# Kernel tuning notes

Measured on AMD Instinct MI355X. Metric: run time of the kernel, lower is better.

## Reference

```python
import jax, jax.numpy as jnp
import numpy as np

N = 100000      # nodes
E = 800000      # edges (nnz of sparse adj)
D_IN = 128      # input feature dim
H = 64          # hidden_units
EMB = 32        # embsize
N_IDX = 50000   # gathered output rows
EPS = 1e-05     # BatchNormalization epsilon


def spmm(rows, cols, vals, x):
    # out[i] = sum_{e: rows[e]==i} vals[e] * x[cols[e]]  == sparse A @ x
    return jax.ops.segment_sum(vals[:, None] * x[cols], rows, num_segments=N)


def batchnorm(x, gamma, beta):
    # training-mode BN over node (batch) axis, matching Keras BatchNormalization
    m = jnp.mean(x, axis=0)
    v = jnp.var(x, axis=0)
    return (x - m) * jax.lax.rsqrt(v + EPS) * gamma + beta


def setup_inputs() -> dict:
    key = jax.random.key(0)
    ks = jax.random.split(key, 16)
    def w(k, fan_in, shape):
        return jax.random.normal(k, shape, dtype=jnp.float32) / np.sqrt(fan_in)
    inp = {
        "features": jax.random.normal(ks[0], (N, D_IN), dtype=jnp.float32),
        "rows": jax.random.randint(ks[1], (E,), 0, N),
        "cols": jax.random.randint(ks[2], (E,), 0, N),
        "vals": jax.random.uniform(ks[3], (E,), dtype=jnp.float32),
        "idx": jax.random.randint(ks[4], (N_IDX,), 0, N),
        # layer 0 (Dense with bias since l==0)
        "Wn0": w(ks[5], D_IN, (D_IN, H)), "bn0": jnp.zeros((H,), jnp.float32),
        "Wg0": w(ks[6], D_IN, (D_IN, H)), "bg0": jnp.zeros((H,), jnp.float32),
        "ab0": jnp.zeros((H,), jnp.float32),  # BiasLayer after SpMM
        "g0": jnp.ones((H,), jnp.float32), "b0": jnp.zeros((H,), jnp.float32),
        # layer 1 (no Dense bias)
        "Wn1": w(ks[7], H, (H, H)),
        "Wg1": w(ks[8], H, (H, H)),
        "ab1": jnp.zeros((H,), jnp.float32),
        "g1": jnp.ones((H,), jnp.float32), "b1": jnp.zeros((H,), jnp.float32),
        # conv_last block (Dense use_bias=False)
        "WnL": w(ks[9], H, (H, EMB)),
        "WgL": w(ks[10], H, (H, EMB)),
        "abL": jnp.zeros((EMB,), jnp.float32),
    }
    return inp


def reference(features, rows, cols, vals, idx,
              Wn0, bn0, Wg0, bg0, ab0, g0, b0,
              Wn1, Wg1, ab1, g1, b1,
              WnL, WgL, abL):
    x = features
    # SAGE layer 0
    x_node = x @ Wn0 + bn0
    x_neigh = x @ Wg0 + bg0
    agg = spmm(rows, cols, vals, x_neigh) + ab0
    x = jax.nn.relu(batchnorm(x_node + agg, g0, b0))
    # SAGE layer 1
    x_node = x @ Wn1
    x_neigh = x @ Wg1
    agg = spmm(rows, cols, vals, x_neigh) + ab1
    x = jax.nn.relu(batchnorm(x_node + agg, g1, b1))
    # conv_last projection to embsize
    x_node = x @ WnL
    x_neigh = x @ WgL
    agg = spmm(rows, cols, vals, x_neigh) + abL
    x = x_node + agg
    return x[idx]
```

## Files before the change

kernel.cpp:

```cpp
#include <hip/hip_runtime.h>

#define NNODES 100000
#define NEDGES 800000
#define DIN    128
#define HID    64
#define EMB    32
#define NIDX   50000
#define BN_EPS 1e-5f

#define NCHK 64
#define EC   (NEDGES / NCHK)
#define NB   ((NNODES + 63) / 64)
#define PF   16
#define NBF  ((NB + PF - 1) / PF)

typedef __attribute__((ext_vector_type(8))) short short8;
typedef __attribute__((ext_vector_type(4))) float f32x4;

__device__ inline unsigned short f2bf(float f) {
    unsigned u = __float_as_uint(f);
    unsigned r = u + 0x7FFFu + ((u >> 16) & 1u);
    return (unsigned short)(r >> 16);
}
__device__ inline float bf2f_lo(unsigned u) { return __uint_as_float(u << 16); }
__device__ inline float bf2f_hi(unsigned u) { return __uint_as_float(u & 0xffff0000u); }


__device__ inline void pack_seg(const float* __restrict__ Wn, const float* __restrict__ Wg,
                                unsigned short* __restrict__ Wp, int HOUT, int l2nt, int f) {
    int j = f & 7, lane = (f >> 3) & 63, g = f >> 9;
    int tt = g & ((1 << l2nt) - 1), kb = g >> l2nt;
    int k = kb * 32 + ((lane >> 4) * 8) + j;
    int nn = tt * 16 + (lane & 15);
    float v = (nn < HOUT) ? Wn[k * HOUT + nn] : Wg[k * HOUT + (nn - HOUT)];
    Wp[f] = f2bf(v);
}


__global__ __launch_bounds__(256) void histpack_k(
    const int* __restrict__ rows, int* __restrict__ Bcnt4, int* __restrict__ bTot,
    const int* __restrict__ idx, int* __restrict__ mark,
    const float* Wn0, const float* Wg0, const float* Wn1,
    const float* Wg1, const float* WnL, const float* WgL,
    unsigned short* Wp0, unsigned short* Wp1, unsigned short* WpL, int MB)
{
    int blk = blockIdx.x;
    int t = threadIdx.x;
    if (blk >= NCHK + MB) {
        int f = (blk - NCHK - MB) * 256 + t;
        if (f < 16384)      pack_seg(Wn0, Wg0, Wp0, 64, 3, f);
        else if (f < 24576) pack_seg(Wn1, Wg1, Wp1, 64, 3, f - 16384);
        else if (f < 28672) pack_seg(WnL, WgL, WpL, 32, 2, f - 24576);
        return;
    }
    if (blk >= NCHK) {
        int j = (blk - NCHK) * 256 + t;
        if (j < NIDX) mark[idx[j]] = 1;
        return;
    }
    __shared__ int hist[NB];
    for (int b = t; b < NB; b += 256) hist[b] = 0;
    __syncthreads();
    const int* rbase = rows + blk * EC;
    for (int i4 = t; i4 < EC / 4; i4 += 256) {
        int4 r4 = *(const int4*)&rbase[i4 * 4];
        atomicAdd(&hist[r4.x >> 6], 1);
        atomicAdd(&hist[r4.y >> 6], 1);
        atomicAdd(&hist[r4.z >> 6], 1);
        atomicAdd(&hist[r4.w >> 6], 1);
    }
    __syncthreads();
    for (int b = t; b < NB; b += 256) {
        int h = hist[b];
        Bcnt4[blk * NB + b] = h;
        if (h) atomicAdd(&bTot[b], h);
    }
}

__global__ __launch_bounds__(256) void scan_k(
    const int* __restrict__ Bcnt4, int* __restrict__ BcntT,
    const int* __restrict__ bTot, int* __restrict__ bBase)
{
    int t = threadIdx.x;
    if (blockIdx.x < 7) {
        int b = blockIdx.x * 256 + t;
        if (b >= NB) return;
        int run = 0;
        for (int c = 0; c < NCHK; c++) {
            BcntT[c * NB + b] = run;
            run += Bcnt4[c * NB + b];
        }
        return;
    }
    __shared__ int s[256];
    int v[7], loc = 0;
#pragma unroll
    for (int i = 0; i < 7; i++) {
        int ix = t * 7 + i;
        v[i] = loc;
        loc += (ix < NB) ? bTot[ix] : 0;
    }
    s[t] = loc;
    __syncthreads();
    for (int off = 1; off < 256; off <<= 1) {
        int a = (t >= off) ? s[t - off] : 0;
        __syncthreads();
        s[t] += a;
        __syncthreads();
    }
    int base = s[t] - loc;
#pragma unroll
    for (int i = 0; i < 7; i++) {
        int ix = t * 7 + i;
        if (ix < NB) bBase[ix] = base + v[i];
    }
    if (t == 255) bBase[NB] = NEDGES;
}


__global__ __launch_bounds__(256) void bfinal_spmm0_k(
    const uint2* __restrict__ ebuf, const int* __restrict__ bBase,
    int* __restrict__ rowptr, int2* __restrict__ cs,
    const unsigned short* __restrict__ Hgb, unsigned short* __restrict__ S,
    float* __restrict__ stats, int n)
{
    __shared__ int hist[64], sc[64], cur[64];
    __shared__ float rs[16][HID], rq[16][HID];
    int b = blockIdx.x, t = threadIdx.x;
    int e0 = bBase[b], e1 = bBase[b + 1];
    int r0 = b << 6;
    if (t < 64) hist[t] = 0;
    __syncthreads();
    for (int i = e0 + t; i < e1; i += 256)
        atomicAdd(&hist[(ebuf[i].x >> 20) & 63], 1);
    __syncthreads();
    if (t == 0) {
        int run = e0;
        for (int j = 0; j < 64; j++) { sc[j] = run; run += hist[j]; }
    }
    __syncthreads();
    if (t < 64) {
        cur[t] = sc[t];
        int r = r0 + t;
        if (r < NNODES) rowptr[r] = sc[t];
    }
    if (b == NB - 1 && t == 0) rowptr[NNODES] = NEDGES;
    __syncthreads();
    for (int i = e0 + t; i < e1; i += 256) {
        uint2 v = ebuf[i];
        int p = atomicAdd(&cur[(v.x >> 20) & 63], 1);
        cs[p] = make_int2((int)(v.x & 0xFFFFF), (int)v.y);
    }
    __syncthreads();

    const int lane = t & 15, g = t >> 4;
    const int c0 = lane * 4;
    float4 sum = make_float4(0.f, 0.f, 0.f, 0.f);
    float4 sq  = make_float4(0.f, 0.f, 0.f, 0.f);
#pragma unroll
    for (int rr = 0; rr < 4; rr++) {
        int lr = g * 4 + rr;
        int row = r0 + lr;
        if (row >= n) break;
        int le0 = sc[lr], le1 = sc[lr] + hist[lr];
        uint2 h = *(const uint2*)&S[(size_t)row * HID + c0];
        float4 a0 = make_float4(bf2f_lo(h.x), bf2f_hi(h.x), bf2f_lo(h.y), bf2f_hi(h.y));
        float4 a1 = make_float4(0.f, 0.f, 0.f, 0.f), a2 = a1, a3 = a1;
        int e = le0;
        for (; e + 3 < le1; e += 4) {
            int2 p0 = cs[e], p1 = cs[e + 1], p2 = cs[e + 2], p3 = cs[e + 3];
            float v0 = __int_as_float(p0.y), v1 = __int_as_float(p1.y);
            float v2 = __int_as_float(p2.y), v3 = __int_as_float(p3.y);
            uint2 h0 = *(const uint2*)&Hgb[(size_t)p0.x * HID + c0];
            uint2 h1 = *(const uint2*)&Hgb[(size_t)p1.x * HID + c0];
            uint2 h2 = *(const uint2*)&Hgb[(size_t)p2.x * HID + c0];
            uint2 h3 = *(const uint2*)&Hgb[(size_t)p3.x * HID + c0];
            a0.x += v0 * bf2f_lo(h0.x); a0.y += v0 * bf2f_hi(h0.x);
            a0.z += v0 * bf2f_lo(h0.y); a0.w += v0 * bf2f_hi(h0.y);
            a1.x += v1 * bf2f_lo(h1.x); a1.y += v1 * bf2f_hi(h1.x);
            a1.z += v1 * bf2f_lo(h1.y); a1.w += v1 * bf2f_hi(h1.y);
            a2.x += v2 * bf2f_lo(h2.x); a2.y += v2 * bf2f_hi(h2.x);
            a2.z += v2 * bf2f_lo(h2.y); a2.w += v2 * bf2f_hi(h2.y);
            a3.x += v3 * bf2f_lo(h3.x); a3.y += v3 * bf2f_hi(h3.x);
            a3.z += v3 * bf2f_lo(h3.y); a3.w += v3 * bf2f_hi(h3.y);
        }
        for (; e < le1; e++) {
            int2 p = cs[e];
            float v = __int_as_float(p.y);
            uint2 hh = *(const uint2*)&Hgb[(size_t)p.x * HID + c0];
            a0.x += v * bf2f_lo(hh.x); a0.y += v * bf2f_hi(hh.x);
            a0.z += v * bf2f_lo(hh.y); a0.w += v * bf2f_hi(hh.y);
        }
        float4 acc = make_float4(a0.x + a1.x + a2.x + a3.x, a0.y + a1.y + a2.y + a3.y,
                                 a0.z + a1.z + a2.z + a3.z, a0.w + a1.w + a2.w + a3.w);
        uint2 o;
        o.x = (unsigned)f2bf(acc.x) | ((unsigned)f2bf(acc.y) << 16);
        o.y = (unsigned)f2bf(acc.z) | ((unsigned)f2bf(acc.w) << 16);
        *(uint2*)&S[(size_t)row * HID + c0] = o;
        sum.x += acc.x; sum.y += acc.y; sum.z += acc.z; sum.w += acc.w;
        sq.x += acc.x * acc.x; sq.y += acc.y * acc.y;
        sq.z += acc.z * acc.z; sq.w += acc.w * acc.w;
    }

    *(float4*)&rs[g][c0] = sum;
    *(float4*)&rq[g][c0] = sq;
    __syncthreads();
    if (t < HID) {
        float a = 0.f, bb = 0.f;
        for (int w = 0; w < 16; w++) { a += rs[w][t]; bb += rq[w][t]; }
        int stripe = b & 7;
        atomicAdd(&stats[stripe * 128 + t], a);
        atomicAdd(&stats[stripe * 128 + HID + t], bb);
    }
}


template <int K, int HOUT, bool AFF, bool XBF, bool HNBF>
__device__ void gemm_body(const void* __restrict__ Xv, const unsigned short* __restrict__ Wp,
                          const float* __restrict__ bnA, const float* __restrict__ bnB,
                          const float* __restrict__ bgA,
                          const float* __restrict__ sums, const float* __restrict__ gamma,
                          const float* __restrict__ beta,
                          float* __restrict__ Hnf, unsigned short* __restrict__ Hnb,
                          unsigned short* __restrict__ Hgb, int n, int blk)
{
    constexpr int NT = 2 * HOUT / 16, NKB = K / 32;
    constexpr int RS = K + 8;
    constexpr int OC = HNBF ? 2 * HOUT : HOUT;
    constexpr int RSE = OC + 8;
    constexpr int XSZ = (RS > RSE) ? RS : RSE;
    __shared__ unsigned short Xs[64 * XSZ];
    __shared__ float sSc[64], sSh[64];

    const int row0 = blk * 64;
    const int t = threadIdx.x;

    if (AFF) {
        if (t < 64) {
            float sum = 0.f, sq = 0.f;
#pragma unroll
            for (int s = 0; s < 8; s++) { sum += sums[s * 128 + t]; sq += sums[s * 128 + 64 + t]; }
            float m = sum / (float)NNODES;
            float var = sq / (float)NNODES - m * m;
            float sc = gamma[t] * rsqrtf(var + BN_EPS);
            sSc[t] = sc; sSh[t] = beta[t] - m * sc;
        }
        __syncthreads();
    }

    constexpr int SIT = K / 32;
    if constexpr (XBF) {
        uint4 u[SIT];
#pragma unroll
        for (int it = 0; it < SIT; it++) {
            int li = it * 256 + t;
            int rr = row0 + li / (K / 8);
            int k8 = (li % (K / 8)) * 8;
            int rc = rr < n ? rr : n - 1;
            u[it] = *(const uint4*)((const unsigned short*)Xv + (size_t)rc * K + k8);
        }
#pragma unroll
        for (int it = 0; it < SIT; it++) {
            int li = it * 256 + t;
            int r  = li / (K / 8);
            int k8 = (li % (K / 8)) * 8;
            float v[8];
            v[0] = bf2f_lo(u[it].x); v[1] = bf2f_hi(u[it].x);
            v[2] = bf2f_lo(u[it].y); v[3] = bf2f_hi(u[it].y);
            v[4] = bf2f_lo(u[it].z); v[5] = bf2f_hi(u[it].z);
            v[6] = bf2f_lo(u[it].w); v[7] = bf2f_hi(u[it].w);
            if (AFF) {
#pragma unroll
                for (int i = 0; i < 8; i++) v[i] = fmaxf(v[i] * sSc[k8 + i] + sSh[k8 + i], 0.f);
            }
            uint4 o;
            o.x = (unsigned)f2bf(v[0]) | ((unsigned)f2bf(v[1]) << 16);
            o.y = (unsigned)f2bf(v[2]) | ((unsigned)f2bf(v[3]) << 16);
            o.z = (unsigned)f2bf(v[4]) | ((unsigned)f2bf(v[5]) << 16);
            o.w = (unsigned)f2bf(v[6]) | ((unsigned)f2bf(v[7]) << 16);
            *(uint4*)&Xs[r * RS + k8] = o;
        }
    } else {
        const float* Xf = (const float*)Xv;
        float4 a[SIT], b[SIT];
#pragma unroll
        for (int it = 0; it < SIT; it++) {
            int li = it * 256 + t;
            int rr = row0 + li / (K / 8);
            int k8 = (li % (K / 8)) * 8;
            int rc = rr < n ? rr : n - 1;
            a[it] = *(const float4*)&Xf[(size_t)rc * K + k8];
            b[it] = *(const float4*)&Xf[(size_t)rc * K + k8 + 4];
        }
#pragma unroll
        for (int it = 0; it < SIT; it++) {
            int li = it * 256 + t;
            int r  = li / (K / 8);
            int k8 = (li % (K / 8)) * 8;
            float v[8] = { a[it].x, a[it].y, a[it].z, a[it].w,
                           b[it].x, b[it].y, b[it].z, b[it].w };
            if (AFF) {
#pragma unroll
                for (int i = 0; i < 8; i++) v[i] = fmaxf(v[i] * sSc[k8 + i] + sSh[k8 + i], 0.f);
            }
            uint4 o;
            o.x = (unsigned)f2bf(v[0]) | ((unsigned)f2bf(v[1]) << 16);
            o.y = (unsigned)f2bf(v[2]) | ((unsigned)f2bf(v[3]) << 16);
            o.z = (unsigned)f2bf(v[4]) | ((unsigned)f2bf(v[5]) << 16);
            o.w = (unsigned)f2bf(v[6]) | ((unsigned)f2bf(v[7]) << 16);
            *(uint4*)&Xs[r * RS + k8] = o;
        }
    }
    __syncthreads();

    const int wave = t >> 6, lane = t & 63;
    const int q = lane >> 4, mrow = lane & 15;

    f32x4 acc[NT];
#pragma unroll
    for (int i = 0; i < NT; i++) acc[i] = (f32x4){0.f, 0.f, 0.f, 0.f};

    const short8* wp8 = (const short8*)Wp;
#pragma unroll
    for (int kb = 0; kb < NKB; kb++) {
        short8 va = *(const short8*)&Xs[(wave * 16 + mrow) * RS + kb * 32 + q * 8];
#pragma unroll
        for (int tt = 0; tt < NT; tt++) {
            short8 vb = wp8[(kb * NT + tt) * 64 + lane];
            acc[tt] = __builtin_amdgcn_mfma_f32_16x16x32_bf16(va, vb, acc[tt], 0, 0, 0);
        }
    }

    __syncthreads();
#pragma unroll
    for (int tt = 0; tt < NT; tt++) {
        int nglob = tt * 16 + mrow;
        bool nside = (nglob < HOUT);
        int c = nside ? nglob : (nglob - HOUT);
        float bias = 0.f;
        if (nside) {
            if (bnA) bias += bnA[c];
            if (bnB) bias += bnB[c];
        } else if (bgA) {
            bias += bgA[c];
        }
        if (HNBF || !nside) {
            int cc = HNBF ? nglob : c;
#pragma unroll
            for (int r = 0; r < 4; r++)
                Xs[(wave * 16 + q * 4 + r) * RSE + cc] = f2bf(acc[tt][r] + bias);
        } else {
#pragma unroll
            for (int r = 0; r < 4; r++) {
                int rr = row0 + wave * 16 + q * 4 + r;
                if (rr < n) Hnf[(size_t)rr * HOUT + c] = acc[tt][r] + bias;
            }
        }
    }
    __syncthreads();
    constexpr int J = OC / 8;
#pragma unroll
    for (int u2 = 0; u2 < (64 * J) / 256; u2++) {
        int li = u2 * 256 + t;
        int r = li / J, j = li % J;
        int rr = row0 + r;
        if (rr < n) {
            uint4 v = *(const uint4*)&Xs[r * RSE + j * 8];
            int c8 = j * 8;
            if (HNBF && c8 < HOUT)
                *(uint4*)&Hnb[(size_t)rr * HOUT + c8] = v;
            else
                *(uint4*)&Hgb[(size_t)rr * HOUT + (HNBF ? c8 - HOUT : c8)] = v;
        }
    }
}

__global__ __launch_bounds__(256) void part_gemm0_k(
    const int* __restrict__ rows, const int* __restrict__ cols,
    const float* __restrict__ vals, const int* __restrict__ BcntT,
    const int* __restrict__ bBase, uint2* __restrict__ ebuf,
    const float* __restrict__ X, const unsigned short* __restrict__ Wp0,
    const float* __restrict__ bn0, const float* __restrict__ ab0, const float* __restrict__ bg0,
    unsigned short* __restrict__ Hn0b, unsigned short* __restrict__ Hgb, int n)
{
    if ((int)blockIdx.x < NCHK * PF) {
        __shared__ int cur[NBF];
        int t = threadIdx.x;
        int blk = blockIdx.x % NCHK;
        int pf  = blockIdx.x / NCHK;
        int b0 = pf * NBF, b1 = (pf == PF - 1) ? NB : (b0 + NBF);
        for (int b = b0 + t; b < b1; b += 256)
            cur[b - b0] = bBase[b] + BcntT[blk * NB + b];
        __syncthreads();
        constexpr int EC4 = EC / 4;
        const int*   rbase = rows + blk * EC;
        const int*   cbase = cols + blk * EC;
        const float* vbase = vals + blk * EC;
        for (int i4 = t; i4 < EC4; i4 += 256) {
            int4   r4 = *(const int4*)&rbase[i4 * 4];
            int4   c4 = *(const int4*)&cbase[i4 * 4];
            float4 v4 = *(const float4*)&vbase[i4 * 4];
#pragma unroll
            for (int j = 0; j < 4; j++) {
                int r = (&r4.x)[j];
                int b = r >> 6;
                if (b >= b0 && b < b1) {
                    int p = atomicAdd(&cur[b - b0], 1);
                    ebuf[p] = make_uint2(((unsigned)(r & 63) << 20) | (unsigned)(&c4.x)[j],
                                         (unsigned)__float_as_int((&v4.x)[j]));
                }
            }
        }
    } else {
        gemm_body<DIN, HID, false, false, true>(X, Wp0, bn0, ab0, bg0,
            nullptr, nullptr, nullptr, nullptr, Hn0b, Hgb, n, blockIdx.x - NCHK * PF);
    }
}

template <int K, int HOUT, bool AFF, bool XBF, bool HNBF>
__global__ __launch_bounds__(256) void gemm_k(
    const void* __restrict__ X, const unsigned short* __restrict__ Wp,
    const float* __restrict__ bnA, const float* __restrict__ bnB, const float* __restrict__ bgA,
    const float* __restrict__ sums, const float* __restrict__ gamma, const float* __restrict__ beta,
    float* __restrict__ Hnf, unsigned short* __restrict__ Hnb, unsigned short* __restrict__ Hgb, int n)
{
    gemm_body<K, HOUT, AFF, XBF, HNBF>(X, Wp, bnA, bnB, bgA, sums, gamma, beta,
                                       Hnf, Hnb, Hgb, n, blockIdx.x);
}


template <int HH, bool STATS, bool SBF, bool MARKED>
__global__ __launch_bounds__(256) void spmm_k(
    const int* __restrict__ rowptr, const int2* __restrict__ cs,
    const unsigned short* __restrict__ Hgb, void* __restrict__ Sv,
    float* __restrict__ stats, const int* __restrict__ mark, int n)
{
    constexpr int L   = HH / 4;
    constexpr int GP  = 256 / L;
    constexpr int RPB = 64;
    constexpr int RPG = RPB / GP;
    constexpr int ECAP = 1024;
    __shared__ int2 es[ECAP];
    __shared__ int  rp[RPB + 1];

    const int t = threadIdx.x;
    const int R0 = blockIdx.x * RPB;
    if (t <= RPB) rp[t] = rowptr[min(R0 + t, n)];
    __syncthreads();
    const int e0b  = rp[0];
    const int scnt = min(rp[RPB] - e0b, ECAP);
    for (int i = t; i < scnt; i += 256) es[i] = cs[e0b + i];
    __syncthreads();

    const int lane = t % L;
    const int g    = t / L;
    const int c0   = lane * 4;

    float4 sum = make_float4(0.f, 0.f, 0.f, 0.f);
    float4 sq  = make_float4(0.f, 0.f, 0.f, 0.f);

#define SPMM_ROW(FETCH)                                                            \
    {                                                                              \
        int e = le0;                                                               \
        for (; e + 3 < le1; e += 4) {                                              \
            int2 p0 = FETCH(e), p1 = FETCH(e + 1), p2 = FETCH(e + 2), p3 = FETCH(e + 3); \
            float v0 = __int_as_float(p0.y), v1 = __int_as_float(p1.y);            \
            float v2 = __int_as_float(p2.y), v3 = __int_as_float(p3.y);            \
            uint2 h0 = *(const uint2*)&Hgb[(size_t)p0.x * HH + c0];                \
            uint2 h1 = *(const uint2*)&Hgb[(size_t)p1.x * HH + c0];                \
            uint2 h2 = *(const uint2*)&Hgb[(size_t)p2.x * HH + c0];                \
            uint2 h3 = *(const uint2*)&Hgb[(size_t)p3.x * HH + c0];                \
            a0.x += v0 * bf2f_lo(h0.x); a0.y += v0 * bf2f_hi(h0.x);                \
            a0.z += v0 * bf2f_lo(h0.y); a0.w += v0 * bf2f_hi(h0.y);                \
            a1.x += v1 * bf2f_lo(h1.x); a1.y += v1 * bf2f_hi(h1.x);                \
            a1.z += v1 * bf2f_lo(h1.y); a1.w += v1 * bf2f_hi(h1.y);                \
            a2.x += v2 * bf2f_lo(h2.x); a2.y += v2 * bf2f_hi(h2.x);                \
            a2.z += v2 * bf2f_lo(h2.y); a2.w += v2 * bf2f_hi(h2.y);                \
            a3.x += v3 * bf2f_lo(h3.x); a3.y += v3 * bf2f_hi(h3.x);                \
            a3.z += v3 * bf2f_lo(h3.y); a3.w += v3 * bf2f_hi(h3.y);                \
        }                                                                          \
        for (; e < le1; e++) {                                                     \
            int2 p = FETCH(e);                                                     \
            float v = __int_as_float(p.y);                                         \
            uint2 h = *(const uint2*)&Hgb[(size_t)p.x * HH + c0];                  \
            a0.x += v * bf2f_lo(h.x); a0.y += v * bf2f_hi(h.x);                    \
            a0.z += v * bf2f_lo(h.y); a0.w += v * bf2f_hi(h.y);                    \
        }                                                                          \
    }
#define F_LDS(i) es[(i)]
#define F_GLB(i) cs[e0b + (i)]

#pragma unroll
    for (int rr = 0; rr < RPG; rr++) {
        int row = R0 + g * RPG + rr;
        if (row >= n) break;
        if (MARKED && !mark[row]) continue;
        int le0 = rp[g * RPG + rr] - e0b;
        int le1 = rp[g * RPG + rr + 1] - e0b;
        float4 a0, a1, a2, a3;
        if (SBF) {
            uint2 h = *(const uint2*)((const unsigned short*)Sv + (size_t)row * HH + c0);
            a0 = make_float4(bf2f_lo(h.x), bf2f_hi(h.x), bf2f_lo(h.y), bf2f_hi(h.y));
        } else {
            a0 = *(const float4*)((const float*)Sv + (size_t)row * HH + c0);
        }
        a1 = a2 = a3 = make_float4(0.f, 0.f, 0.f, 0.f);
        if (le1 <= scnt) SPMM_ROW(F_LDS) else SPMM_ROW(F_GLB);
        float4 acc = make_float4(a0.x + a1.x + a2.x + a3.x, a0.y + a1.y + a2.y + a3.y,
                                 a0.z + a1.z + a2.z + a3.z, a0.w + a1.w + a2.w + a3.w);
        if (SBF) {
            uint2 o;
            o.x = (unsigned)f2bf(acc.x) | ((unsigned)f2bf(acc.y) << 16);
            o.y = (unsigned)f2bf(acc.z) | ((unsigned)f2bf(acc.w) << 16);
            *(uint2*)((unsigned short*)Sv + (size_t)row * HH + c0) = o;
        } else {
            *(float4*)((float*)Sv + (size_t)row * HH + c0) = acc;
        }
        if (STATS) {
            sum.x += acc.x; sum.y += acc.y; sum.z += acc.z; sum.w += acc.w;
            sq.x += acc.x * acc.x; sq.y += acc.y * acc.y;
            sq.z += acc.z * acc.z; sq.w += acc.w * acc.w;
        }
    }
#undef SPMM_ROW
#undef F_LDS
#undef F_GLB

    if constexpr (STATS) {
        __shared__ float rs[GP][HH];
        __shared__ float rq[GP][HH];
        *(float4*)&rs[g][c0] = sum;
        *(float4*)&rq[g][c0] = sq;
        __syncthreads();
        if (threadIdx.x < HH) {
            float a = 0.f, b = 0.f;
            for (int w = 0; w < GP; w++) { a += rs[w][threadIdx.x]; b += rq[w][threadIdx.x]; }
            int stripe = blockIdx.x & 7;
            atomicAdd(&stats[stripe * 128 + threadIdx.x], a);
            atomicAdd(&stats[stripe * 128 + HH + threadIdx.x], b);
        }
    }
}

__global__ void gather_k(const float* __restrict__ S, const int* __restrict__ idx,
                         float* __restrict__ out, int total4) {
    int j = blockIdx.x * 256 + threadIdx.x;
    if (j < total4) {
        int r = j / (EMB / 4), c4 = (j % (EMB / 4)) * 4;
        *(float4*)&out[(size_t)j * 4] = *(const float4*)&S[(size_t)idx[r] * EMB + c4];
    }
}


extern "C" void kernel_launch(void* const* d_in, const int* in_sizes, int n_in,
                              void* d_out, int out_size, void* d_ws, size_t ws_size,
                              hipStream_t stream) {
    const float* features = (const float*)d_in[0];
    const int*   rows     = (const int*)d_in[1];
    const int*   cols     = (const int*)d_in[2];
    const float* vals     = (const float*)d_in[3];
    const int*   idx      = (const int*)d_in[4];
    const float* Wn0 = (const float*)d_in[5];
    const float* bn0 = (const float*)d_in[6];
    const float* Wg0 = (const float*)d_in[7];
    const float* bg0 = (const float*)d_in[8];
    const float* ab0 = (const float*)d_in[9];
    const float* g0  = (const float*)d_in[10];
    const float* b0  = (const float*)d_in[11];
    const float* Wn1 = (const float*)d_in[12];
    const float* Wg1 = (const float*)d_in[13];
    const float* ab1 = (const float*)d_in[14];
    const float* g1  = (const float*)d_in[15];
    const float* b1  = (const float*)d_in[16];
    const float* WnL = (const float*)d_in[17];
    const float* WgL = (const float*)d_in[18];
    const float* abL = (const float*)d_in[19];
    float* out = (float*)d_out;

    float*          HnLf = (float*)d_ws;
    unsigned short* nA   = (unsigned short*)(HnLf + (size_t)NNODES * EMB);
    unsigned short* nB   = nA + (size_t)NNODES * HID;
    unsigned short* Hgb  = nB + (size_t)NNODES * HID;
    uint2* ebuf  = (uint2*)(Hgb + (size_t)NNODES * HID);
    int2*  cs    = (int2*)(ebuf + NEDGES);
    int*   rowptr = (int*)(cs + NEDGES);
    int*   Bcnt4 = rowptr + (NNODES + 4);
    int*   BcntT = Bcnt4 + NCHK * NB;
    int*   bBase = BcntT + NCHK * NB;
    unsigned short* Wp0 = (unsigned short*)(bBase + 1568);
    unsigned short* Wp1 = Wp0 + 16384;
    unsigned short* WpL = Wp1 + 8192;
    float* stats = (float*)(WpL + 4096);
    int*   mark  = (int*)(stats + 2304);
    int*   bTot  = mark + NNODES;
    float* sums0 = stats;
    float* sums1 = stats + 1024;
    size_t zbytes = 2304 * 4 + (size_t)NNODES * 4 + 1568 * 4;

    hipMemsetAsync(stats, 0, zbytes, stream);

    const int GBm = (NNODES + 63) / 64;
    const int MB  = (NIDX + 255) / 256;

    histpack_k<<<NCHK + MB + 112, 256, 0, stream>>>(
        rows, Bcnt4, bTot, idx, mark, Wn0, Wg0, Wn1, Wg1, WnL, WgL, Wp0, Wp1, WpL, MB);
    scan_k<<<8, 256, 0, stream>>>(Bcnt4, BcntT, bTot, bBase);
    part_gemm0_k<<<NCHK * PF + GBm, 256, 0, stream>>>(rows, cols, vals, BcntT, bBase, ebuf,
                                                      features, Wp0, bn0, ab0, bg0,
                                                      nA, Hgb, NNODES);
    bfinal_spmm0_k<<<NB, 256, 0, stream>>>(ebuf, bBase, rowptr, cs, Hgb, nA, sums0, NNODES);

    gemm_k<HID, HID, true, true, true><<<GBm, 256, 0, stream>>>(
        nA, Wp1, ab1, nullptr, nullptr, sums0, g0, b0, nullptr, nB, Hgb, NNODES);
    spmm_k<HID, true, true, false><<<GBm, 256, 0, stream>>>(rowptr, cs, Hgb, nB, sums1, nullptr, NNODES);

    gemm_k<HID, EMB, true, true, false><<<GBm, 256, 0, stream>>>(
        nB, WpL, abL, nullptr, nullptr, sums1, g1, b1, HnLf, nullptr, Hgb, NNODES);
    spmm_k<EMB, false, false, true><<<GBm, 256, 0, stream>>>(rowptr, cs, Hgb, HnLf, nullptr, mark, NNODES);

    gather_k<<<(NIDX * EMB / 4 + 255) / 256, 256, 0, stream>>>(HnLf, idx, out, NIDX * EMB / 4);
}
```

Measured before the change: 258.0 us.

## Stage bucket edges in registers and LDS for CSR build and SpMM0

The bucket-finalize kernel now loads each block's edges into registers once, reusing them for both the histogram and scatter passes instead of reading ebuf twice. The scattered column/value pairs go into a 1024-entry LDS buffer, which the fused layer-0 SpMM then reads directly rather than re-reading cs from global memory. The global cs copy is still written for later layers. Separately, the edge-partition loop software-prefetches the next int4 row/col/val batch before processing the current one. The extra 8KB of LDS and the added registers may reduce occupancy.

```diff
diff --git a/kernel.cpp b/kernel.cpp
--- a/kernel.cpp
+++ b/kernel.cpp
@@ -124,39 +124,66 @@
     const unsigned short* __restrict__ Hgb, unsigned short* __restrict__ S,
     float* __restrict__ stats, int n)
 {
+    constexpr int ECAP = 1024;
     __shared__ int hist[64], sc[64], cur[64];
+    __shared__ int2 es2[ECAP];
     __shared__ float rs[16][HID], rq[16][HID];
     int b = blockIdx.x, t = threadIdx.x;
     int e0 = bBase[b], e1 = bBase[b + 1];
+    int cnt = e1 - e0;
     int r0 = b << 6;
     if (t < 64) hist[t] = 0;
     __syncthreads();
-    for (int i = e0 + t; i < e1; i += 256)
-        atomicAdd(&hist[(ebuf[i].x >> 20) & 63], 1);
+
+    uint2 ev0, ev1, ev2, ev3;
+    bool h0 = t < cnt, h1 = t + 256 < cnt, h2 = t + 512 < cnt, h3 = t + 768 < cnt;
+    if (h0) { ev0 = ebuf[e0 + t];       atomicAdd(&hist[(ev0.x >> 20) & 63], 1); }
+    if (h1) { ev1 = ebuf[e0 + t + 256]; atomicAdd(&hist[(ev1.x >> 20) & 63], 1); }
+    if (h2) { ev2 = ebuf[e0 + t + 512]; atomicAdd(&hist[(ev2.x >> 20) & 63], 1); }
+    if (h3) { ev3 = ebuf[e0 + t + 768]; atomicAdd(&hist[(ev3.x >> 20) & 63], 1); }
+    for (int i = t + ECAP; i < cnt; i += 256) {
+        uint2 v = ebuf[e0 + i];
+        atomicAdd(&hist[(v.x >> 20) & 63], 1);
+    }
     __syncthreads();
     if (t == 0) {
-        int run = e0;
+        int run = 0;
         for (int j = 0; j < 64; j++) { sc[j] = run; run += hist[j]; }
     }
     __syncthreads();
     if (t < 64) {
         cur[t] = sc[t];
         int r = r0 + t;
-        if (r < NNODES) rowptr[r] = sc[t];
+        if (r < NNODES) rowptr[r] = e0 + sc[t];
     }
     if (b == NB - 1 && t == 0) rowptr[NNODES] = NEDGES;
     __syncthreads();
-    for (int i = e0 + t; i < e1; i += 256) {
-        uint2 v = ebuf[i];
-        int p = atomicAdd(&cur[(v.x >> 20) & 63], 1);
-        cs[p] = make_int2((int)(v.x & 0xFFFFF), (int)v.y);
-    }
-    __syncthreads();
+
+#define SCAT(V)                                                          \
+    {                                                                    \
+        int p = atomicAdd(&cur[((V).x >> 20) & 63], 1);                  \
+        int2 pay = make_int2((int)((V).x & 0xFFFFF), (int)(V).y);        \
+        if (p < ECAP) es2[p] = pay; else cs[e0 + p] = pay;               \
+    }
+    if (h0) SCAT(ev0)
+    if (h1) SCAT(ev1)
+    if (h2) SCAT(ev2)
+    if (h3) SCAT(ev3)
+    for (int i = t + ECAP; i < cnt; i += 256) {
+        uint2 v = ebuf[e0 + i];
+        SCAT(v)
+    }
+#undef SCAT
+    __syncthreads();
+
+    int scnt = min(cnt, ECAP);
+    for (int i = t; i < scnt; i += 256) cs[e0 + i] = es2[i];
 
     const int lane = t & 15, g = t >> 4;
     const int c0 = lane * 4;
     float4 sum = make_float4(0.f, 0.f, 0.f, 0.f);
     float4 sq  = make_float4(0.f, 0.f, 0.f, 0.f);
+#define FE(i) ((i) < ECAP ? es2[(i)] : cs[e0 + (i)])
 #pragma unroll
     for (int rr = 0; rr < 4; rr++) {
         int lr = g * 4 + rr;
@@ -168,24 +195,24 @@
         float4 a1 = make_float4(0.f, 0.f, 0.f, 0.f), a2 = a1, a3 = a1;
         int e = le0;
         for (; e + 3 < le1; e += 4) {
-            int2 p0 = cs[e], p1 = cs[e + 1], p2 = cs[e + 2], p3 = cs[e + 3];
+            int2 p0 = FE(e), p1 = FE(e + 1), p2 = FE(e + 2), p3 = FE(e + 3);
             float v0 = __int_as_float(p0.y), v1 = __int_as_float(p1.y);
             float v2 = __int_as_float(p2.y), v3 = __int_as_float(p3.y);
-            uint2 h0 = *(const uint2*)&Hgb[(size_t)p0.x * HID + c0];
-            uint2 h1 = *(const uint2*)&Hgb[(size_t)p1.x * HID + c0];
-            uint2 h2 = *(const uint2*)&Hgb[(size_t)p2.x * HID + c0];
-            uint2 h3 = *(const uint2*)&Hgb[(size_t)p3.x * HID + c0];
-            a0.x += v0 * bf2f_lo(h0.x); a0.y += v0 * bf2f_hi(h0.x);
-            a0.z += v0 * bf2f_lo(h0.y); a0.w += v0 * bf2f_hi(h0.y);
-            a1.x += v1 * bf2f_lo(h1.x); a1.y += v1 * bf2f_hi(h1.x);
-            a1.z += v1 * bf2f_lo(h1.y); a1.w += v1 * bf2f_hi(h1.y);
-            a2.x += v2 * bf2f_lo(h2.x); a2.y += v2 * bf2f_hi(h2.x);
-            a2.z += v2 * bf2f_lo(h2.y); a2.w += v2 * bf2f_hi(h2.y);
-            a3.x += v3 * bf2f_lo(h3.x); a3.y += v3 * bf2f_hi(h3.x);
-            a3.z += v3 * bf2f_lo(h3.y); a3.w += v3 * bf2f_hi(h3.y);
+            uint2 h0v = *(const uint2*)&Hgb[(size_t)p0.x * HID + c0];
+            uint2 h1v = *(const uint2*)&Hgb[(size_t)p1.x * HID + c0];
+            uint2 h2v = *(const uint2*)&Hgb[(size_t)p2.x * HID + c0];
+            uint2 h3v = *(const uint2*)&Hgb[(size_t)p3.x * HID + c0];
+            a0.x += v0 * bf2f_lo(h0v.x); a0.y += v0 * bf2f_hi(h0v.x);
+            a0.z += v0 * bf2f_lo(h0v.y); a0.w += v0 * bf2f_hi(h0v.y);
+            a1.x += v1 * bf2f_lo(h1v.x); a1.y += v1 * bf2f_hi(h1v.x);
+            a1.z += v1 * bf2f_lo(h1v.y); a1.w += v1 * bf2f_hi(h1v.y);
+            a2.x += v2 * bf2f_lo(h2v.x); a2.y += v2 * bf2f_hi(h2v.x);
+            a2.z += v2 * bf2f_lo(h2v.y); a2.w += v2 * bf2f_hi(h2v.y);
+            a3.x += v3 * bf2f_lo(h3v.x); a3.y += v3 * bf2f_hi(h3v.x);
+            a3.z += v3 * bf2f_lo(h3v.y); a3.w += v3 * bf2f_hi(h3v.y);
         }
         for (; e < le1; e++) {
-            int2 p = cs[e];
+            int2 p = FE(e);
             float v = __int_as_float(p.y);
             uint2 hh = *(const uint2*)&Hgb[(size_t)p.x * HID + c0];
             a0.x += v * bf2f_lo(hh.x); a0.y += v * bf2f_hi(hh.x);
@@ -201,6 +228,7 @@
         sq.x += acc.x * acc.x; sq.y += acc.y * acc.y;
         sq.z += acc.z * acc.z; sq.w += acc.w * acc.w;
     }
+#undef FE
 
     *(float4*)&rs[g][c0] = sum;
     *(float4*)&rq[g][c0] = sq;
@@ -396,20 +424,32 @@
         const int*   rbase = rows + blk * EC;
         const int*   cbase = cols + blk * EC;
         const float* vbase = vals + blk * EC;
-        for (int i4 = t; i4 < EC4; i4 += 256) {
-            int4   r4 = *(const int4*)&rbase[i4 * 4];
-            int4   c4 = *(const int4*)&cbase[i4 * 4];
-            float4 v4 = *(const float4*)&vbase[i4 * 4];
+        int i4 = t;
+        int4 r4, c4; float4 v4;
+        if (i4 < EC4) {
+            r4 = *(const int4*)&rbase[i4 * 4];
+            c4 = *(const int4*)&cbase[i4 * 4];
+            v4 = *(const float4*)&vbase[i4 * 4];
+        }
+        while (i4 < EC4) {
+            int4 rr = r4; int4 cc = c4; float4 vv = v4;
+            int ni = i4 + 256;
+            if (ni < EC4) {
+                r4 = *(const int4*)&rbase[ni * 4];
+                c4 = *(const int4*)&cbase[ni * 4];
+                v4 = *(const float4*)&vbase[ni * 4];
+            }
 #pragma unroll
             for (int j = 0; j < 4; j++) {
-                int r = (&r4.x)[j];
+                int r = (&rr.x)[j];
                 int b = r >> 6;
                 if (b >= b0 && b < b1) {
                     int p = atomicAdd(&cur[b - b0], 1);
-                    ebuf[p] = make_uint2(((unsigned)(r & 63) << 20) | (unsigned)(&c4.x)[j],
-                                         (unsigned)__float_as_int((&v4.x)[j]));
+                    ebuf[p] = make_uint2(((unsigned)(r & 63) << 20) | (unsigned)(&cc.x)[j],
+                                         (unsigned)__float_as_int((&vv.x)[j]));
                 }
             }
+            i4 = ni;
         }
     } else {
         gemm_body<DIN, HID, false, false, true>(X, Wp0, bn0, ab0, bg0,
```

New measurement: 252.4 us, median of 3. -2.2%, faster.
